# Optimization experiments

Measured on AMD Instinct MI355X. Metric: run time of the kernel, lower is better.

Reference implementation:

```python
import jax, jax.numpy as jnp
import numpy as np

INPUT, HIDDEN = 8, 16

def setup_inputs() -> dict:
    key = jax.random.key(0)
    ks = jax.random.split(key, 7)
    s_ih = 1.0 / np.sqrt(HIDDEN)
    x = jax.random.normal(ks[0], (8192, 512, INPUT), dtype=jnp.float32)
    W_ih = jax.random.uniform(ks[1], (HIDDEN, INPUT), jnp.float32, -s_ih, s_ih)
    W_hh = jax.random.uniform(ks[2], (HIDDEN, HIDDEN), jnp.float32, -s_ih, s_ih)
    b_ih = jax.random.uniform(ks[3], (HIDDEN,), jnp.float32, -s_ih, s_ih)
    b_hh = jax.random.uniform(ks[4], (HIDDEN,), jnp.float32, -s_ih, s_ih)
    s_fc = 1.0 / np.sqrt(HIDDEN)
    fc_w = jax.random.uniform(ks[5], (1, HIDDEN), jnp.float32, -s_fc, s_fc)
    fc_b = jax.random.uniform(ks[6], (1,), jnp.float32, -s_fc, s_fc)
    return {"x": x, "W_ih": W_ih, "W_hh": W_hh, "b_ih": b_ih, "b_hh": b_hh, "fc_w": fc_w, "fc_b": fc_b}

def reference(x, W_ih, W_hh, b_ih, b_hh, fc_w, fc_b):
    B, T, _ = x.shape
    # Precompute input projection for all timesteps: [B, T, H]
    xp = jnp.einsum('bti,hi->bth', x, W_ih) + b_ih + b_hh
    h0 = jnp.zeros((B, HIDDEN), dtype=x.dtype)

    def step(h, xt):
        h_new = jnp.tanh(xt + h @ W_hh.T)
        return h_new, None

    h_last, _ = jax.lax.scan(step, h0, jnp.swapaxes(xp, 0, 1))
    return h_last @ fc_w.T + fc_b  # [B, 1]
```

## Files before the change

### kernel.cpp

```cpp
#include <hip/hip_runtime.h>


#define RNN_B   8192
#define RNN_T   512
#define RNN_IN  8
#define RNN_H   16
#define TC      32
#define NB      16
#define XSTRIDE 264
#define HP      20

__global__ __launch_bounds__(256, 2) void rnn_fused_kernel(
    const float* __restrict__ x,
    const float* __restrict__ W_ih,
    const float* __restrict__ W_hh,
    const float* __restrict__ b_ih,
    const float* __restrict__ b_hh,
    const float* __restrict__ fc_w,
    const float* __restrict__ fc_b,
    float* __restrict__ out)
{
    __shared__ float xs[NB * XSTRIDE];
    __shared__ float hbuf[NB * HP];

    const int tid = (int)threadIdx.x;
    const int j   = tid & 15;
    const int g   = tid >> 4;
    const int b0  = (int)blockIdx.x * NB;
    const int b   = b0 + g;

    float whh[RNN_H];
#pragma unroll
    for (int k = 0; k < RNN_H; k += 4) {
        float4 w = *(const float4*)(W_hh + j * RNN_H + k);
        whh[k] = w.x; whh[k+1] = w.y; whh[k+2] = w.z; whh[k+3] = w.w;
    }
    float wih[RNN_IN];
#pragma unroll
    for (int i = 0; i < RNN_IN; i += 4) {
        float4 w = *(const float4*)(W_ih + j * RNN_IN + i);
        wih[i] = w.x; wih[i+1] = w.y; wih[i+2] = w.z; wih[i+3] = w.w;
    }
    const float bias = b_ih[j] + b_hh[j];

    hbuf[g * HP + j] = 0.0f;

    float hlast = 0.0f;

    for (int t0 = 0; t0 < RNN_T; t0 += TC) {
        __syncthreads();
#pragma unroll
        for (int p = 0; p < 4; ++p) {
            int idx = tid + p * 256;
            int row = idx >> 6;
            int off = idx & 63;
            float4 v = *(const float4*)(x + ((size_t)(b0 + row) * RNN_T + t0) * RNN_IN + off * 4);
            *(float4*)(xs + row * XSTRIDE + off * 4) = v;
        }
        __syncthreads();

#pragma unroll 4
        for (int tt = 0; tt < TC; ++tt) {
            const float* xp = xs + g * XSTRIDE + tt * RNN_IN;
            const float4 xa = *(const float4*)(xp);
            const float4 xb = *(const float4*)(xp + 4);
            const float4 h0 = *(const float4*)(hbuf + g * HP + 0);
            const float4 h1 = *(const float4*)(hbuf + g * HP + 4);
            const float4 h2 = *(const float4*)(hbuf + g * HP + 8);
            const float4 h3 = *(const float4*)(hbuf + g * HP + 12);

            float a0 = fmaf(wih[0], xa.x, bias);
            a0 = fmaf(wih[1], xa.y, a0);
            a0 = fmaf(wih[2], xa.z, a0);
            a0 = fmaf(wih[3], xa.w, a0);
            a0 = fmaf(whh[0], h0.x, a0);
            a0 = fmaf(whh[1], h0.y, a0);

            float a1 = wih[4] * xb.x;
            a1 = fmaf(wih[5], xb.y, a1);
            a1 = fmaf(wih[6], xb.z, a1);
            a1 = fmaf(wih[7], xb.w, a1);
            a1 = fmaf(whh[2], h0.z, a1);
            a1 = fmaf(whh[3], h0.w, a1);

            float a2 = whh[4] * h1.x;
            a2 = fmaf(whh[5],  h1.y, a2);
            a2 = fmaf(whh[6],  h1.z, a2);
            a2 = fmaf(whh[7],  h1.w, a2);
            a2 = fmaf(whh[8],  h2.x, a2);
            a2 = fmaf(whh[9],  h2.y, a2);

            float a3 = whh[10] * h2.z;
            a3 = fmaf(whh[11], h2.w, a3);
            a3 = fmaf(whh[12], h3.x, a3);
            a3 = fmaf(whh[13], h3.y, a3);
            a3 = fmaf(whh[14], h3.z, a3);
            a3 = fmaf(whh[15], h3.w, a3);

            const float s = (a0 + a1) + (a2 + a3);

            const float e  = __expf(s + s);
            const float r  = __builtin_amdgcn_rcpf(e + 1.0f);
            const float hn = fmaf(-2.0f, r, 1.0f);

            hbuf[g * HP + j] = hn;
            hlast = hn;
        }
    }

    float v = hlast * fc_w[j];
    v += __shfl_xor(v, 1);
    v += __shfl_xor(v, 2);
    v += __shfl_xor(v, 4);
    v += __shfl_xor(v, 8);
    if (j == 0) out[b] = v + fc_b[0];
}

extern "C" void kernel_launch(void* const* d_in, const int* in_sizes, int n_in,
                              void* d_out, int out_size, void* d_ws, size_t ws_size,
                              hipStream_t stream)
{
    const float* x    = (const float*)d_in[0];
    const float* W_ih = (const float*)d_in[1];
    const float* W_hh = (const float*)d_in[2];
    const float* b_ih = (const float*)d_in[3];
    const float* b_hh = (const float*)d_in[4];
    const float* fc_w = (const float*)d_in[5];
    const float* fc_b = (const float*)d_in[6];
    float* out = (float*)d_out;

    dim3 grid(RNN_B / NB);
    dim3 block(256);
    rnn_fused_kernel<<<grid, block, 0, stream>>>(x, W_ih, W_hh, b_ih, b_hh, fc_w, fc_b, out);
}
```

Measured before the change: 239.5 us.

## Exchange hidden state across lanes with DPP row rotations instead of LDS

The recurrent hidden state now stays in registers, one element per lane. Each lane gathers the other fifteen elements through DPP row-rotate operations, with the W_hh row pre-permuted to match the rotation order. This removes the per-step shared-memory write and reload from the serial recurrence's critical path. The unroll factor is also raised. The cost is fifteen cross-lane moves per step, which may or may not fold into the FMAs.

```diff
diff --git a/kernel.cpp b/kernel.cpp
--- a/kernel.cpp
+++ b/kernel.cpp
@@ -8,7 +8,12 @@
 #define TC      32
 #define NB      16
 #define XSTRIDE 264
-#define HP      20
+
+template<int R>
+__device__ __forceinline__ float ror16(float v) {
+    return __int_as_float(__builtin_amdgcn_update_dpp(
+        0, __float_as_int(v), 0x120 + R, 0xF, 0xF, false));
+}
 
 __global__ __launch_bounds__(256, 2) void rnn_fused_kernel(
     const float* __restrict__ x,
@@ -21,7 +26,6 @@
     float* __restrict__ out)
 {
     __shared__ float xs[NB * XSTRIDE];
-    __shared__ float hbuf[NB * HP];
 
     const int tid = (int)threadIdx.x;
     const int j   = tid & 15;
@@ -29,11 +33,10 @@
     const int b0  = (int)blockIdx.x * NB;
     const int b   = b0 + g;
 
-    float whh[RNN_H];
+    float wperm[RNN_H];
 #pragma unroll
-    for (int k = 0; k < RNN_H; k += 4) {
-        float4 w = *(const float4*)(W_hh + j * RNN_H + k);
-        whh[k] = w.x; whh[k+1] = w.y; whh[k+2] = w.z; whh[k+3] = w.w;
+    for (int r = 0; r < RNN_H; ++r) {
+        wperm[r] = W_hh[j * RNN_H + ((j - r) & 15)];
     }
     float wih[RNN_IN];
 #pragma unroll
@@ -43,9 +46,7 @@
     }
     const float bias = b_ih[j] + b_hh[j];
 
-    hbuf[g * HP + j] = 0.0f;
-
-    float hlast = 0.0f;
+    float h = 0.0f;
 
     for (int t0 = 0; t0 < RNN_T; t0 += TC) {
         __syncthreads();
@@ -59,56 +60,48 @@
         }
         __syncthreads();
 
-#pragma unroll 4
+#pragma unroll 8
         for (int tt = 0; tt < TC; ++tt) {
             const float* xp = xs + g * XSTRIDE + tt * RNN_IN;
             const float4 xa = *(const float4*)(xp);
             const float4 xb = *(const float4*)(xp + 4);
-            const float4 h0 = *(const float4*)(hbuf + g * HP + 0);
-            const float4 h1 = *(const float4*)(hbuf + g * HP + 4);
-            const float4 h2 = *(const float4*)(hbuf + g * HP + 8);
-            const float4 h3 = *(const float4*)(hbuf + g * HP + 12);
 
             float a0 = fmaf(wih[0], xa.x, bias);
             a0 = fmaf(wih[1], xa.y, a0);
             a0 = fmaf(wih[2], xa.z, a0);
             a0 = fmaf(wih[3], xa.w, a0);
-            a0 = fmaf(whh[0], h0.x, a0);
-            a0 = fmaf(whh[1], h0.y, a0);
 
             float a1 = wih[4] * xb.x;
             a1 = fmaf(wih[5], xb.y, a1);
             a1 = fmaf(wih[6], xb.z, a1);
             a1 = fmaf(wih[7], xb.w, a1);
-            a1 = fmaf(whh[2], h0.z, a1);
-            a1 = fmaf(whh[3], h0.w, a1);
 
-            float a2 = whh[4] * h1.x;
-            a2 = fmaf(whh[5],  h1.y, a2);
-            a2 = fmaf(whh[6],  h1.z, a2);
-            a2 = fmaf(whh[7],  h1.w, a2);
-            a2 = fmaf(whh[8],  h2.x, a2);
-            a2 = fmaf(whh[9],  h2.y, a2);
-
-            float a3 = whh[10] * h2.z;
-            a3 = fmaf(whh[11], h2.w, a3);
-            a3 = fmaf(whh[12], h3.x, a3);
-            a3 = fmaf(whh[13], h3.y, a3);
-            a3 = fmaf(whh[14], h3.z, a3);
-            a3 = fmaf(whh[15], h3.w, a3);
+            float a2 = wperm[0] * h;
+            float a3 = wperm[1] * ror16<1>(h);
+            a0 = fmaf(wperm[2],  ror16<2>(h),  a0);
+            a1 = fmaf(wperm[3],  ror16<3>(h),  a1);
+            a2 = fmaf(wperm[4],  ror16<4>(h),  a2);
+            a3 = fmaf(wperm[5],  ror16<5>(h),  a3);
+            a0 = fmaf(wperm[6],  ror16<6>(h),  a0);
+            a1 = fmaf(wperm[7],  ror16<7>(h),  a1);
+            a2 = fmaf(wperm[8],  ror16<8>(h),  a2);
+            a3 = fmaf(wperm[9],  ror16<9>(h),  a3);
+            a0 = fmaf(wperm[10], ror16<10>(h), a0);
+            a1 = fmaf(wperm[11], ror16<11>(h), a1);
+            a2 = fmaf(wperm[12], ror16<12>(h), a2);
+            a3 = fmaf(wperm[13], ror16<13>(h), a3);
+            a0 = fmaf(wperm[14], ror16<14>(h), a0);
+            a1 = fmaf(wperm[15], ror16<15>(h), a1);
 
             const float s = (a0 + a1) + (a2 + a3);
 
-            const float e  = __expf(s + s);
-            const float r  = __builtin_amdgcn_rcpf(e + 1.0f);
-            const float hn = fmaf(-2.0f, r, 1.0f);
-
-            hbuf[g * HP + j] = hn;
-            hlast = hn;
+            const float e = __expf(s + s);
+            const float r = __builtin_amdgcn_rcpf(e + 1.0f);
+            h = fmaf(-2.0f, r, 1.0f);
         }
     }
 
-    float v = hlast * fc_w[j];
+    float v = h * fc_w[j];
     v += __shfl_xor(v, 1);
     v += __shfl_xor(v, 2);
     v += __shfl_xor(v, 4);
```

Measured after the change: 269.4 us. 1.12x slower.
